# Kernel optimization log

Measured on AMD Instinct MI355X. Metric: run time of the kernel, lower is better.

## Reference

```python
import math
import jax, jax.numpy as jnp
import numpy as np

NUM_CLUSTERS = 512
KMEANS_ITERS = 3
TOLERANCE = 1e-4
N_SAMPLES = 131072
EMB_DIM = 128


def setup_inputs() -> dict:
    key = jax.random.key(0)
    data = jax.random.normal(key, (N_SAMPLES, EMB_DIM), dtype=jnp.float32)
    return {"data": data}


def _cdist(x, y):
    # Euclidean distance matrix [N, K], matching torch.cdist (p=2).
    x2 = jnp.sum(x * x, axis=-1, keepdims=True)          # [N,1]
    y2 = jnp.sum(y * y, axis=-1)                          # [K]
    sq = x2 + y2 - 2.0 * (x @ y.T)
    return jnp.sqrt(jnp.maximum(sq, 0.0))


def _assign_clusters(dist, num_clusters, max_per_cluster):
    # Capacity-constrained greedy assignment, sequential over samples
    # (faithful to the original double loop), expressed as a lax.scan.
    sorted_idx = jnp.argsort(dist, axis=-1)               # [N, K]

    def step(counts, row):
        avail = counts[row] < max_per_cluster             # [K] in preference order
        pos = jnp.argmax(avail)                           # first available cluster
        chosen = jnp.where(jnp.any(avail), row[pos], jnp.argmin(counts))
        counts = counts.at[chosen].add(1)
        return counts, chosen

    counts0 = jnp.zeros((num_clusters,), dtype=jnp.int32)
    _, labels = jax.lax.scan(step, counts0, sorted_idx)
    return labels                                         # [N] int32


def _update_codebook(data, labels, old_codebook, num_clusters):
    sums = jax.ops.segment_sum(data, labels, num_segments=num_clusters)  # [K,d]
    cnt = jax.ops.segment_sum(jnp.ones((data.shape[0],), data.dtype),
                              labels, num_segments=num_clusters)          # [K]
    means = sums / jnp.maximum(cnt, 1.0)[:, None]
    # Empty clusters keep their old centroid.
    return jnp.where(cnt[:, None] > 0, means, old_codebook)


def _fit(data):
    n, _ = data.shape
    k = NUM_CLUSTERS
    cap = math.ceil(n / k)  # static python int
    # Init: random subset of rows (num_emb >= num_clusters path).
    perm = jax.random.permutation(jax.random.key(42), n)[:k]
    codebook0 = data[perm]

    def kmeans_iter(carry, _):
        cb, labels, done = carry
        dist = _cdist(data, cb)
        new_labels = _assign_clusters(dist, k, cap)
        new_cb = _update_codebook(data, new_labels, cb, k)
        converged = jnp.linalg.norm(new_cb - cb) < TOLERANCE
        cb_out = jnp.where(done, cb, new_cb)
        labels_out = jnp.where(done, labels, new_labels)
        return (cb_out, labels_out, jnp.logical_or(done, converged)), None

    init = (codebook0, jnp.zeros((n,), jnp.int32), jnp.array(False))
    (codebook, labels, _), _ = jax.lax.scan(kmeans_iter, init, None,
                                            length=KMEANS_ITERS)
    return codebook, labels


def reference(data):
    # Returns (codebook [K,d], samples_labels [N]) like BalancedKmeans.fit.
    return _fit(data)
```

## Files before the change

kernel.cpp:

```cpp
#include <hip/hip_runtime.h>
#include <cstdint>
#include <cstring>
#include <vector>

#define RNG_PARTITIONABLE 1

#define NS 131072
#define D  128
#define KC 512
#define CAPC 256
#define TS 32

static constexpr size_t OFF_YT    = 0;
static constexpr size_t OFF_Y2    = OFF_YT + (size_t)D * KC * 8;
static constexpr size_t OFF_CB    = OFF_Y2 + (size_t)KC * 8;
static constexpr size_t OFF_NORM  = OFF_CB + (size_t)KC * D * 4;
static constexpr size_t OFF_DONE  = OFF_NORM + 8;
static constexpr size_t OFF_SCAL  = OFF_DONE + 4;
static constexpr size_t OFF_CNT   = OFF_SCAL + 12;
static constexpr size_t OFF_OPENL = OFF_CNT + (size_t)KC * 4;
static constexpr size_t OFF_MCNT  = OFF_OPENL + (size_t)KC * 2;
static constexpr size_t OFF_MEMB  = OFF_MCNT + (size_t)KC * 4;
static constexpr size_t OFF_LBL   = OFF_MEMB + (size_t)KC * CAPC * 4;
static constexpr size_t OFF_SL    = ((OFF_LBL + (size_t)NS * 4 + 15) / 16) * 16;

struct PermArg { uint32_t v[KC]; };

__device__ inline unsigned long long sortkey(double d) {
  unsigned long long u = (unsigned long long)__double_as_longlong(d);
  return (u & 0x8000000000000000ull) ? ~u : (u | 0x8000000000000000ull);
}

__device__ inline double dot128(const float* __restrict__ x, const float* __restrict__ y) {
  double s0 = 0, s1 = 0, s2 = 0, s3 = 0;
#pragma unroll
  for (int k = 0; k < D; k += 4) {
    float4 a = *reinterpret_cast<const float4*>(x + k);
    float4 b = *reinterpret_cast<const float4*>(y + k);
    s0 = fma((double)a.x, (double)b.x, s0);
    s1 = fma((double)a.y, (double)b.y, s1);
    s2 = fma((double)a.z, (double)b.z, s2);
    s3 = fma((double)a.w, (double)b.w, s3);
  }
  return (s0 + s1) + (s2 + s3);
}

__device__ inline void bitonic64(unsigned long long& k, uint32_t& v, int lane) {
#pragma unroll
  for (int sz = 2; sz <= 64; sz <<= 1) {
#pragma unroll
    for (int st = sz >> 1; st > 0; st >>= 1) {
      unsigned long long ok = __shfl_xor(k, st);
      uint32_t ov = __shfl_xor(v, st);
      bool dirAsc = ((lane & sz) == 0);
      bool low = ((lane & st) == 0);
      bool oless = (ok < k) || (ok == k && ov < v);
      bool take = (dirAsc == low) ? oless : !oless;
      if (take) { k = ok; v = ov; }
    }
  }
}

__global__ void k_init(uint32_t* done) {
  if (threadIdx.x == 0 && blockIdx.x == 0) *done = 0u;
}

__global__ void k_gather(PermArg p, const float* __restrict__ data, float* __restrict__ cb) {
  int c = blockIdx.x, t = threadIdx.x;
  cb[(size_t)c * D + t] = data[(size_t)p.v[c] * D + t];
}

__global__ __launch_bounds__(64) void k_prep(const float* __restrict__ cb,
    double* __restrict__ yT, double* __restrict__ y2g, const uint32_t* __restrict__ done) {
  if (*done) return;
  const int c = blockIdx.x;
  const int lane = threadIdx.x;
  double v0 = (double)cb[(size_t)c * D + lane];
  double v1 = (double)cb[(size_t)c * D + 64 + lane];
  yT[(size_t)lane * KC + c] = v0;
  yT[(size_t)(lane + 64) * KC + c] = v1;
  double q = fma(v0, v0, v1 * v1);
  for (int d2 = 32; d2; d2 >>= 1) q += __shfl_xor(q, d2);
  if (lane == 0) y2g[c] = q;
}

__global__ __launch_bounds__(256) void k_dist(const float* __restrict__ data,
    const double* __restrict__ yT, const double* __restrict__ y2g,
    uint16_t* __restrict__ sl, const uint32_t* __restrict__ done) {
  if (*done) return;
  __shared__ double xs[16][D];
  __shared__ uint32_t hist[256];
  __shared__ unsigned long long candK[64];
  __shared__ uint32_t candI[64];
  __shared__ uint32_t candCnt;
  __shared__ double redMn[4], redMx[4];
  __shared__ double sKey[4];
  __shared__ int sId[4];
  __shared__ int cutSh;
  __shared__ uint32_t totSh;
  __shared__ int winSh;

  const int tid = threadIdx.x;
  const int lane = tid & 63;
  const int wv = tid >> 6;
  const int rowBase = blockIdx.x * 16;

  for (int idx = tid; idx < 16 * D; idx += 256) {
    int r = idx >> 7, k = idx & 127;
    xs[r][k] = (double)data[(size_t)(rowBase + r) * D + k];
  }
  __syncthreads();

  const int c0 = tid, c1 = tid + 256;
  double acc0[16], acc1[16];
#pragma unroll
  for (int r = 0; r < 16; ++r) { acc0[r] = 0.0; acc1[r] = 0.0; }

  for (int k = 0; k < D; ++k) {
    double yv0 = yT[(size_t)k * KC + c0];
    double yv1 = yT[(size_t)k * KC + c1];
#pragma unroll
    for (int r = 0; r < 16; ++r) {
      double xv = xs[r][k];
      acc0[r] = fma(xv, yv0, acc0[r]);
      acc1[r] = fma(xv, yv1, acc1[r]);
    }
  }
  {
    double y20 = y2g[c0], y21 = y2g[c1];
#pragma unroll
    for (int r = 0; r < 16; ++r) {
      acc0[r] = fma(-2.0, acc0[r], y20);
      acc1[r] = fma(-2.0, acc1[r], y21);
    }
  }

#pragma unroll
  for (int r = 0; r < 16; ++r) {
    const double v0 = acc0[r], v1 = acc1[r];
    double mn = fmin(v0, v1), mx = fmax(v0, v1);
    for (int d2 = 32; d2; d2 >>= 1) {
      mn = fmin(mn, __shfl_xor(mn, d2));
      mx = fmax(mx, __shfl_xor(mx, d2));
    }
    if (lane == 0) { redMn[wv] = mn; redMx[wv] = mx; }
    __syncthreads();
    mn = fmin(fmin(redMn[0], redMn[1]), fmin(redMn[2], redMn[3]));
    mx = fmax(fmax(redMx[0], redMx[1]), fmax(redMx[2], redMx[3]));
    double rng = mx - mn;
    double inv = (rng > 0.0) ? (255.0 / rng) : 0.0;
    hist[tid] = 0;
    if (tid == 0) candCnt = 0;
    __syncthreads();
    int b0 = (int)((v0 - mn) * inv); b0 = b0 < 0 ? 0 : (b0 > 255 ? 255 : b0);
    int b1 = (int)((v1 - mn) * inv); b1 = b1 < 0 ? 0 : (b1 > 255 ? 255 : b1);
    atomicAdd(&hist[b0], 1u);
    atomicAdd(&hist[b1], 1u);
    __syncthreads();
    if (wv == 0) {
      uint32_t h0 = hist[lane * 4], h1 = hist[lane * 4 + 1], h2 = hist[lane * 4 + 2], h3 = hist[lane * 4 + 3];
      uint32_t ls = h0 + h1 + h2 + h3, x = ls;
      for (int d2 = 1; d2 < 64; d2 <<= 1) { uint32_t y = __shfl_up(x, d2); if (lane >= d2) x += y; }
      uint32_t e = x - ls;
      uint32_t cA = e + h0, cB = cA + h1, cC = cB + h2, cD = cC + h3;
      int mc = 999; uint32_t mt = 0;
      if (cA >= 32) { mc = lane * 4; mt = cA; }
      else if (cB >= 32) { mc = lane * 4 + 1; mt = cB; }
      else if (cC >= 32) { mc = lane * 4 + 2; mt = cC; }
      else if (cD >= 32) { mc = lane * 4 + 3; mt = cD; }
      for (int d2 = 32; d2; d2 >>= 1) {
        int oc = __shfl_xor(mc, d2); uint32_t ot = __shfl_xor(mt, d2);
        if (oc < mc) { mc = oc; mt = ot; }
      }
      if (lane == 0) { cutSh = mc; totSh = mt; }
    }
    __syncthreads();
    const int cut = cutSh;
    const uint32_t tot = totSh;
    if (tot <= 64u) {
      if (b0 <= cut) { uint32_t s2 = atomicAdd(&candCnt, 1u); candK[s2] = sortkey(v0); candI[s2] = (uint32_t)c0; }
      if (b1 <= cut) { uint32_t s2 = atomicAdd(&candCnt, 1u); candK[s2] = sortkey(v1); candI[s2] = (uint32_t)c1; }
      __syncthreads();
      if (wv == 0) {
        uint32_t nc = candCnt;
        unsigned long long kk = ~0ull; uint32_t id = 0xFFFFu;
        if ((uint32_t)lane < nc) { kk = candK[lane]; id = candI[lane]; }
        bitonic64(kk, id, lane);
        if (lane < TS) sl[(size_t)(rowBase + r) * TS + lane] = (uint16_t)id;
      }
      __syncthreads();
    } else {
      uint32_t tk = 0;
      for (int sel = 0; sel < 32; ++sel) {
        double bv = 1e300; int bc = 0x7FFFFFFF;
        if (!(tk & 1u)) { bv = v0; bc = c0; }
        if (!(tk & 2u) && (v1 < bv || (v1 == bv && c1 < bc))) { bv = v1; bc = c1; }
        for (int d2 = 32; d2; d2 >>= 1) {
          double ov = __shfl_xor(bv, d2); int oc = __shfl_xor(bc, d2);
          if (ov < bv || (ov == bv && oc < bc)) { bv = ov; bc = oc; }
        }
        if (lane == 0) { sKey[wv] = bv; sId[wv] = bc; }
        __syncthreads();
        if (tid == 0) {
          double fb = sKey[0]; int fc = sId[0];
          for (int w2 = 1; w2 < 4; ++w2) {
            if (sKey[w2] < fb || (sKey[w2] == fb && sId[w2] < fc)) { fb = sKey[w2]; fc = sId[w2]; }
          }
          winSh = fc;
          sl[(size_t)(rowBase + r) * TS + sel] = (uint16_t)fc;
        }
        __syncthreads();
        int wc = winSh;
        if (tid == (wc & 255)) tk |= (wc < 256) ? 1u : 2u;
        __syncthreads();
      }
    }
  }
}

__device__ inline int walkstep(const uint4 cc, const uint16_t* __restrict__ sl,
    uint32_t i, int& ptr, const uint32_t* cnt) {
  while (ptr < TS) {
    uint32_t c;
    if (ptr < 8) {
      uint32_t w = (ptr < 4) ? ((ptr < 2) ? cc.x : cc.y) : ((ptr < 6) ? cc.z : cc.w);
      c = (w >> ((ptr & 1) * 16)) & 0xFFFFu;
    } else {
      c = sl[(size_t)i * TS + ptr];
    }
    if (c < KC && cnt[c] < CAPC) return (int)c;
    ++ptr;
  }
  return -1;
}

__device__ inline void resolve_overflow(int& choice, uint32_t i, int lane,
    const uint32_t* cnt, const double* __restrict__ y2g,
    const float* __restrict__ cb, const float* __restrict__ data) {
  unsigned long long om = __ballot(choice < 0);
  while (om) {
    int L = __ffsll(om) - 1;
    om &= om - 1;
    uint32_t iL = __shfl(i, L);
    const float* x = data + (size_t)iL * D;
    double bv = 1e300; int bc = 0x7FFFFFFF;
    for (int j = 0; j < 8; ++j) {
      int c = lane + 64 * j;
      if (cnt[c] < CAPC) {
        double v = y2g[c] - 2.0 * dot128(x, cb + (size_t)c * D);
        if (v < bv || (v == bv && c < bc)) { bv = v; bc = c; }
      }
    }
    for (int d2 = 32; d2; d2 >>= 1) {
      double ov = __shfl_xor(bv, d2); int oc = __shfl_xor(bc, d2);
      if (ov < bv || (ov == bv && oc < bc)) { bv = ov; bc = oc; }
    }
    if (lane == L) choice = bc;
  }
}

__global__ __launch_bounds__(64) void k_ev(const float* __restrict__ data,
    const float* __restrict__ cb, const double* __restrict__ y2g,
    const uint16_t* __restrict__ sl, uint32_t* __restrict__ cntG,
    uint32_t* __restrict__ scal, uint16_t* __restrict__ openLG,
    int* __restrict__ labels, const uint32_t* __restrict__ done,
    int stopOpen, int initFlag) {
  if (*done) return;
  __shared__ uint32_t cnt[KC];
  __shared__ uint32_t hist[KC];
  __shared__ uint32_t reach[96];
  __shared__ uint32_t reachCnt;
  __shared__ uint32_t openSh;
  __shared__ uint32_t posSh;
  __shared__ uint32_t olc;
  const int lane = threadIdx.x;

  if (initFlag) {
    for (int c = lane; c < KC; c += 64) cnt[c] = 0;
    if (lane == 0) { openSh = KC; posSh = 0; }
  } else {
    for (int c = lane; c < KC; c += 64) cnt[c] = cntG[c];
    if (lane == 0) { posSh = scal[0]; openSh = scal[1]; }
  }
  __syncthreads();
  uint32_t pos = posSh;

  uint4 pf0, pf1;
  {
    uint32_t s0 = pos + lane; if (s0 >= NS) s0 = NS - 1;
    uint32_t s1 = pos + 64 + lane; if (s1 >= NS) s1 = NS - 1;
    pf0 = *reinterpret_cast<const uint4*>(sl + (size_t)s0 * TS);
    pf1 = *reinterpret_cast<const uint4*>(sl + (size_t)s1 * TS);
  }

  while (pos < NS) {
    if (openSh <= (uint32_t)stopOpen) break;
    uint32_t i = pos + lane;
    uint4 pf2;
    {
      uint32_t s2i = pos + 128 + lane; if (s2i >= NS) s2i = NS - 1;
      pf2 = *reinterpret_cast<const uint4*>(sl + (size_t)s2i * TS);
    }
    int ptr = 0;
    bool exempt = false;
    int choice = walkstep(pf0, sl, i, ptr, cnt);
    resolve_overflow(choice, i, lane, cnt, y2g, cb, data);

    for (;;) {
      for (int c = lane; c < KC; c += 64) hist[c] = 0;
      if (lane == 0) reachCnt = 0;
      __syncthreads();
      if (!exempt) atomicAdd(&hist[choice], 1u);
      __syncthreads();
      for (int c = lane; c < KC; c += 64) {
        uint32_t cc = cnt[c];
        if (cc < CAPC && cc + hist[c] >= CAPC) {
          uint32_t s2 = atomicAdd(&reachCnt, 1u);
          if (s2 < 96) reach[s2] = c;
        }
      }
      __syncthreads();
      uint32_t nr = reachCnt; if (nr > 96) nr = 96;
      if (nr == 0) break;
      int Lstar = 64;
      for (uint32_t t = 0; t < nr; ++t) {
        uint32_t c = reach[t];
        uint32_t rem = CAPC - cnt[c];
        unsigned long long m = __ballot((!exempt) && choice == (int)c);
        if ((uint32_t)__popcll(m) > rem) {
          unsigned long long mm = m;
          for (uint32_t q = 0; q < rem; ++q) mm &= mm - 1;
          int fi = __ffsll(mm) - 1;
          if (fi < Lstar) Lstar = fi;
        }
      }
      if (Lstar == 64) break;
      bool inval = false;
      for (uint32_t t = 0; t < nr; ++t) {
        uint32_t c = reach[t];
        uint32_t cc = cnt[c];
        if (cc >= CAPC) continue;
        uint32_t rem = CAPC - cc;
        unsigned long long m = __ballot((!exempt) && choice == (int)c);
        uint32_t pc = (uint32_t)__popcll(m);
        if (pc >= rem) {
          unsigned long long mm = m;
          for (uint32_t q = 0; q + 1 < rem; ++q) mm &= mm - 1;
          int fl = __ffsll(mm) - 1;
          if (fl < Lstar) {
            __syncthreads();
            if (lane == 0) { cnt[c] = CAPC; openSh--; }
            __syncthreads();
            if ((!exempt) && choice == (int)c) {
              uint32_t rk = (uint32_t)__popcll(m & ((1ull << lane) - 1ull));
              if (rk < rem) exempt = true; else inval = true;
            }
          }
        }
      }
      __syncthreads();
      if (inval) {
        if (ptr < TS) { ++ptr; choice = walkstep(pf0, sl, i, ptr, cnt); }
        else choice = -1;
      }
      resolve_overflow(choice, i, lane, cnt, y2g, cb, data);
      __syncthreads();
    }
    uint32_t old = 0;
    if (!exempt) old = atomicAdd(&cnt[choice], 1u);
    labels[i] = choice;
    __syncthreads();
    if (!exempt && old == CAPC - 1) atomicSub(&openSh, 1u);
    __syncthreads();
    pos += 64;
    pf0 = pf1; pf1 = pf2;
  }

  __syncthreads();
  for (int c = lane; c < KC; c += 64) cntG[c] = cnt[c];
  if (lane == 0) olc = 0;
  __syncthreads();
  for (int j = 0; j < 8; ++j) {
    int c = lane + 64 * j;
    bool op = cnt[c] < CAPC;
    unsigned long long m = __ballot(op);
    uint32_t base = olc;
    uint32_t rk = (uint32_t)__popcll(m & ((1ull << lane) - 1ull));
    if (op) openLG[base + rk] = (uint16_t)c;
    __syncthreads();
    if (lane == 0) olc += (uint32_t)__popcll(m);
    __syncthreads();
  }
  if (lane == 0) { scal[0] = pos; scal[1] = openSh; scal[2] = olc; }
}

__global__ __launch_bounds__(256) void k_rebuild(const float* __restrict__ data,
    const float* __restrict__ cb, const double* __restrict__ y2g,
    uint16_t* __restrict__ sl, const uint32_t* __restrict__ scal,
    const uint16_t* __restrict__ openLG, const uint32_t* __restrict__ done) {
  if (*done) return;
  uint32_t pos = scal[0];
  if (pos >= NS) return;
  uint32_t oc = scal[2]; if (oc > 64) oc = 64;
  const int lane = threadIdx.x & 63;
  const uint32_t wid = (blockIdx.x * blockDim.x + threadIdx.x) >> 6;
  const uint32_t nw = (gridDim.x * blockDim.x) >> 6;
  int c = -1; double y2v = 0.0; const float* yrow = cb;
  if ((uint32_t)lane < oc) { c = openLG[lane]; y2v = y2g[c]; yrow = cb + (size_t)c * D; }
  for (uint32_t s = pos + wid; s < NS; s += nw) {
    unsigned long long kk = ~0ull; uint32_t id = 0xFFFFu;
    if (c >= 0) {
      double v = y2v - 2.0 * dot128(data + (size_t)s * D, yrow);
      kk = sortkey(v); id = (uint32_t)c;
    }
    bitonic64(kk, id, lane);
    if (lane < TS) sl[(size_t)s * TS + lane] = (uint16_t)id;
  }
}

__global__ void k_zero(uint32_t* mcnt, double* norm) {
  int i = blockIdx.x * blockDim.x + threadIdx.x;
  if (i < KC) mcnt[i] = 0u;
  if (i == 0) *norm = 0.0;
}

__global__ void k_scatter(const int* __restrict__ labels, uint32_t* __restrict__ mcnt,
    uint32_t* __restrict__ memb, const uint32_t* __restrict__ done) {
  if (*done) return;
  uint32_t i = blockIdx.x * blockDim.x + threadIdx.x;
  int c = labels[i];
  if ((unsigned)c < KC) {
    uint32_t s = atomicAdd(&mcnt[c], 1u);
    if (s < CAPC) memb[(size_t)c * CAPC + s] = i;
  }
}

__global__ __launch_bounds__(128) void k_update(const float* __restrict__ data,
    const uint32_t* __restrict__ memb, float* __restrict__ cb,
    double* __restrict__ norm, const uint32_t* __restrict__ done) {
  if (*done) return;
  const int c = blockIdx.x, t = threadIdx.x;
  __shared__ uint32_t mem[CAPC];
  __shared__ double qq[2];
  mem[t] = memb[(size_t)c * CAPC + t] & (NS - 1);
  mem[t + 128] = memb[(size_t)c * CAPC + 128 + t] & (NS - 1);
  __syncthreads();
  double a = 0.0;
  for (int m = 0; m < CAPC; ++m) a += (double)data[(size_t)mem[m] * D + t];
  float nv = (float)(a * (1.0 / 256.0));
  double df = (double)nv - (double)cb[(size_t)c * D + t];
  cb[(size_t)c * D + t] = nv;
  double q = df * df;
  for (int d2 = 32; d2; d2 >>= 1) q += __shfl_xor(q, d2);
  if ((t & 63) == 0) qq[t >> 6] = q;
  __syncthreads();
  if (t == 0) atomicAdd(norm, qq[0] + qq[1]);
}

__global__ void k_conv(const double* __restrict__ norm, uint32_t* __restrict__ done) {
  if (threadIdx.x == 0 && blockIdx.x == 0) {
    if (*norm < 1e-8) *done = 1u;
  }
}

__global__ void k_out(const float* __restrict__ cb, float* __restrict__ o) {
  int i = blockIdx.x * blockDim.x + threadIdx.x;
  o[i] = cb[i];
}

__global__ void k_outL(const int* __restrict__ lbl, float* __restrict__ o) {
  int i = blockIdx.x * blockDim.x + threadIdx.x;
  o[i] = (float)lbl[i];
}

static void tf2x32(uint32_t k0, uint32_t k1, uint32_t x0, uint32_t x1, uint32_t& o0, uint32_t& o1) {
  uint32_t ks2 = k0 ^ k1 ^ 0x1BD11BDAu;
  x0 += k0; x1 += k1;
  auto R = [&](int r) { x0 += x1; x1 = (x1 << r) | (x1 >> (32 - r)); x1 ^= x0; };
  R(13); R(15); R(26); R(6);   x0 += k1;  x1 += ks2 + 1u;
  R(17); R(29); R(16); R(24);  x0 += ks2; x1 += k0 + 2u;
  R(13); R(15); R(26); R(6);   x0 += k0;  x1 += k1 + 3u;
  R(17); R(29); R(16); R(24);  x0 += k1;  x1 += ks2 + 4u;
  R(13); R(15); R(26); R(6);   x0 += ks2; x1 += k0 + 5u;
  o0 = x0; o1 = x1;
}

static void host_sort_kv(std::vector<uint32_t>& k, std::vector<uint32_t>& v) {
  const size_t n = k.size();
  std::vector<uint32_t> k2(n), v2(n);
  for (int sh = 0; sh < 32; sh += 8) {
    uint32_t cnt2[257];
    memset(cnt2, 0, sizeof cnt2);
    for (size_t i = 0; i < n; ++i) cnt2[((k[i] >> sh) & 255u) + 1]++;
    for (int b = 0; b < 256; ++b) cnt2[b + 1] += cnt2[b];
    for (size_t i = 0; i < n; ++i) {
      uint32_t b = (k[i] >> sh) & 255u;
      uint32_t d = cnt2[b]++;
      k2[d] = k[i]; v2[d] = v[i];
    }
    k.swap(k2); v.swap(v2);
  }
}

static void compute_perm(uint32_t* out) {
  const uint32_t n = NS;
  std::vector<uint32_t> vals(n), keys(n);
  for (uint32_t i = 0; i < n; ++i) vals[i] = i;
  uint32_t k0 = 0u, k1 = 42u;
  for (int round = 0; round < 2; ++round) {
    uint32_t nk0, nk1, sk0, sk1;
#if RNG_PARTITIONABLE
    tf2x32(k0, k1, 0u, 0u, nk0, nk1);
    tf2x32(k0, k1, 0u, 1u, sk0, sk1);
    for (uint32_t i = 0; i < n; ++i) {
      uint32_t b1, b2;
      tf2x32(sk0, sk1, 0u, i, b1, b2);
      keys[i] = b1 ^ b2;
    }
#else
    {
      uint32_t a0, b0, a1, b1v;
      tf2x32(k0, k1, 0u, 2u, a0, b0);
      tf2x32(k0, k1, 1u, 3u, a1, b1v);
      nk0 = a0; nk1 = a1; sk0 = b0; sk1 = b1v;
    }
    {
      const uint32_t h = n / 2;
      for (uint32_t i = 0; i < h; ++i) {
        uint32_t o0, o1;
        tf2x32(sk0, sk1, i, i + h, o0, o1);
        keys[i] = o0; keys[i + h] = o1;
      }
    }
#endif
    host_sort_kv(keys, vals);
    k0 = nk0; k1 = nk1;
  }
  memcpy(out, vals.data(), KC * sizeof(uint32_t));
}

extern "C" void kernel_launch(void* const* d_in, const int* in_sizes, int n_in,
                              void* d_out, int out_size, void* d_ws, size_t ws_size,
                              hipStream_t stream) {
  const float* data = (const float*)d_in[0];
  float* outCB = (float*)d_out;
  float* outLB = (float*)d_out + (size_t)KC * D;

  char* w = (char*)d_ws;
  double* yT = (double*)(w + OFF_YT);
  double* y2 = (double*)(w + OFF_Y2);
  float* cb = (float*)(w + OFF_CB);
  double* norm = (double*)(w + OFF_NORM);
  uint32_t* done = (uint32_t*)(w + OFF_DONE);
  uint32_t* scal = (uint32_t*)(w + OFF_SCAL);
  uint32_t* cnt = (uint32_t*)(w + OFF_CNT);
  uint16_t* openL = (uint16_t*)(w + OFF_OPENL);
  uint32_t* mcnt = (uint32_t*)(w + OFF_MCNT);
  uint32_t* memb = (uint32_t*)(w + OFF_MEMB);
  int* lbl = (int*)(w + OFF_LBL);
  uint16_t* sl = (uint16_t*)(w + OFF_SL);

  PermArg pa;
  compute_perm(pa.v);

  k_init<<<1, 64, 0, stream>>>(done);
  k_gather<<<KC, D, 0, stream>>>(pa, data, cb);

  for (int it = 0; it < 3; ++it) {
    k_prep<<<KC, 64, 0, stream>>>(cb, yT, y2, done);
    k_dist<<<NS / 16, 256, 0, stream>>>(data, yT, y2, sl, done);
    k_ev<<<1, 64, 0, stream>>>(data, cb, y2, sl, cnt, scal, openL, lbl, done, 64, 1);
    k_rebuild<<<256, 256, 0, stream>>>(data, cb, y2, sl, scal, openL, done);
    k_ev<<<1, 64, 0, stream>>>(data, cb, y2, sl, cnt, scal, openL, lbl, done, 32, 0);
    k_rebuild<<<256, 256, 0, stream>>>(data, cb, y2, sl, scal, openL, done);
    k_ev<<<1, 64, 0, stream>>>(data, cb, y2, sl, cnt, scal, openL, lbl, done, 0, 0);
    k_zero<<<2, 256, 0, stream>>>(mcnt, norm);
    k_scatter<<<NS / 256, 256, 0, stream>>>(lbl, mcnt, memb, done);
    k_update<<<KC, 128, 0, stream>>>(data, memb, cb, norm, done);
    k_conv<<<1, 64, 0, stream>>>(norm, done);
  }
  k_out<<<KC * D / 256, 256, 0, stream>>>(cb, outCB);
  k_outL<<<NS / 256, 256, 0, stream>>>(lbl, outLB);
}
```

Measured before the change: 125.1 ms.

## Add optimistic fast path to greedy assignment wavefront, deepen prefetch

The sequential assignment kernel now optimistically atomically adds each lane's first-available choice (unrolled check of the 8 prefetched candidates) and only falls back to the histogram/reach conflict-resolution loop if any lane overflowed capacity. Shared-memory scalars (open count, position, list offset) become wave-uniform registers updated by ballot/popcount, removing several __syncthreads per step. The sorted-list prefetch distance is increased from 2 to 5 batches ahead. It adds register pressure and relies on the rollback path being correct when overflow happens.

```diff
diff --git a/kernel.cpp b/kernel.cpp
--- a/kernel.cpp
+++ b/kernel.cpp
@@ -270,128 +270,151 @@
   __shared__ uint32_t hist[KC];
   __shared__ uint32_t reach[96];
   __shared__ uint32_t reachCnt;
-  __shared__ uint32_t openSh;
-  __shared__ uint32_t posSh;
-  __shared__ uint32_t olc;
   const int lane = threadIdx.x;
 
+  uint32_t pos, openCnt;
   if (initFlag) {
     for (int c = lane; c < KC; c += 64) cnt[c] = 0;
-    if (lane == 0) { openSh = KC; posSh = 0; }
+    pos = 0; openCnt = KC;
   } else {
     for (int c = lane; c < KC; c += 64) cnt[c] = cntG[c];
-    if (lane == 0) { posSh = scal[0]; openSh = scal[1]; }
+    pos = scal[0]; openCnt = scal[1];
   }
   __syncthreads();
-  uint32_t pos = posSh;
-
-  uint4 pf0, pf1;
+
+  uint4 p0, p1, p2, p3, p4;
   {
-    uint32_t s0 = pos + lane; if (s0 >= NS) s0 = NS - 1;
-    uint32_t s1 = pos + 64 + lane; if (s1 >= NS) s1 = NS - 1;
-    pf0 = *reinterpret_cast<const uint4*>(sl + (size_t)s0 * TS);
-    pf1 = *reinterpret_cast<const uint4*>(sl + (size_t)s1 * TS);
-  }
-
-  while (pos < NS) {
-    if (openSh <= (uint32_t)stopOpen) break;
-    uint32_t i = pos + lane;
-    uint4 pf2;
+    uint32_t s;
+    s = pos + lane;        if (s >= NS) s = NS - 1; p0 = *reinterpret_cast<const uint4*>(sl + (size_t)s * TS);
+    s = pos + 64 + lane;   if (s >= NS) s = NS - 1; p1 = *reinterpret_cast<const uint4*>(sl + (size_t)s * TS);
+    s = pos + 128 + lane;  if (s >= NS) s = NS - 1; p2 = *reinterpret_cast<const uint4*>(sl + (size_t)s * TS);
+    s = pos + 192 + lane;  if (s >= NS) s = NS - 1; p3 = *reinterpret_cast<const uint4*>(sl + (size_t)s * TS);
+    s = pos + 256 + lane;  if (s >= NS) s = NS - 1; p4 = *reinterpret_cast<const uint4*>(sl + (size_t)s * TS);
+  }
+
+  while (pos < NS && openCnt > (uint32_t)stopOpen) {
+    const uint32_t i = pos + lane;
+    uint4 pN;
     {
-      uint32_t s2i = pos + 128 + lane; if (s2i >= NS) s2i = NS - 1;
-      pf2 = *reinterpret_cast<const uint4*>(sl + (size_t)s2i * TS);
-    }
-    int ptr = 0;
-    bool exempt = false;
-    int choice = walkstep(pf0, sl, i, ptr, cnt);
+      uint32_t s = pos + 320 + lane; if (s >= NS) s = NS - 1;
+      pN = *reinterpret_cast<const uint4*>(sl + (size_t)s * TS);
+    }
+
+    uint32_t e0 = p0.x & 0xFFFFu, e1 = p0.x >> 16, e2 = p0.y & 0xFFFFu, e3 = p0.y >> 16,
+             e4 = p0.z & 0xFFFFu, e5 = p0.z >> 16, e6 = p0.w & 0xFFFFu, e7 = p0.w >> 16;
+    uint32_t q0 = cnt[e0 < KC ? e0 : 0], q1 = cnt[e1 < KC ? e1 : 0],
+             q2 = cnt[e2 < KC ? e2 : 0], q3 = cnt[e3 < KC ? e3 : 0],
+             q4 = cnt[e4 < KC ? e4 : 0], q5 = cnt[e5 < KC ? e5 : 0],
+             q6 = cnt[e6 < KC ? e6 : 0], q7 = cnt[e7 < KC ? e7 : 0];
+    int choice = -1, ptr = TS;
+    if (e7 < KC && q7 < CAPC) { choice = (int)e7; ptr = 7; }
+    if (e6 < KC && q6 < CAPC) { choice = (int)e6; ptr = 6; }
+    if (e5 < KC && q5 < CAPC) { choice = (int)e5; ptr = 5; }
+    if (e4 < KC && q4 < CAPC) { choice = (int)e4; ptr = 4; }
+    if (e3 < KC && q3 < CAPC) { choice = (int)e3; ptr = 3; }
+    if (e2 < KC && q2 < CAPC) { choice = (int)e2; ptr = 2; }
+    if (e1 < KC && q1 < CAPC) { choice = (int)e1; ptr = 1; }
+    if (e0 < KC && q0 < CAPC) { choice = (int)e0; ptr = 0; }
+    if (__ballot(choice < 0)) {
+      if (choice < 0) { ptr = 8; choice = walkstep(p0, sl, i, ptr, cnt); }
+    }
     resolve_overflow(choice, i, lane, cnt, y2g, cb, data);
 
-    for (;;) {
-      for (int c = lane; c < KC; c += 64) hist[c] = 0;
-      if (lane == 0) reachCnt = 0;
+    uint32_t old = atomicAdd(&cnt[choice], 1u);
+    unsigned long long ovf = __ballot(old >= CAPC);
+    if (ovf == 0ull) {
+      labels[i] = choice;
+      unsigned long long fills = __ballot(old == CAPC - 1);
+      openCnt -= (uint32_t)__popcll(fills);
+    } else {
+      atomicSub(&cnt[choice], 1u);
       __syncthreads();
-      if (!exempt) atomicAdd(&hist[choice], 1u);
-      __syncthreads();
-      for (int c = lane; c < KC; c += 64) {
-        uint32_t cc = cnt[c];
-        if (cc < CAPC && cc + hist[c] >= CAPC) {
-          uint32_t s2 = atomicAdd(&reachCnt, 1u);
-          if (s2 < 96) reach[s2] = c;
+      bool exempt = false;
+      for (;;) {
+        for (int c = lane; c < KC; c += 64) hist[c] = 0;
+        if (lane == 0) reachCnt = 0;
+        __syncthreads();
+        if (!exempt) atomicAdd(&hist[choice], 1u);
+        __syncthreads();
+        for (int c = lane; c < KC; c += 64) {
+          uint32_t cc = cnt[c];
+          if (cc < CAPC && cc + hist[c] >= CAPC) {
+            uint32_t s2 = atomicAdd(&reachCnt, 1u);
+            if (s2 < 96) reach[s2] = c;
+          }
         }
-      }
-      __syncthreads();
-      uint32_t nr = reachCnt; if (nr > 96) nr = 96;
-      if (nr == 0) break;
-      int Lstar = 64;
-      for (uint32_t t = 0; t < nr; ++t) {
-        uint32_t c = reach[t];
-        uint32_t rem = CAPC - cnt[c];
-        unsigned long long m = __ballot((!exempt) && choice == (int)c);
-        if ((uint32_t)__popcll(m) > rem) {
-          unsigned long long mm = m;
-          for (uint32_t q = 0; q < rem; ++q) mm &= mm - 1;
-          int fi = __ffsll(mm) - 1;
-          if (fi < Lstar) Lstar = fi;
+        __syncthreads();
+        uint32_t nr = reachCnt; if (nr > 96) nr = 96;
+        if (nr == 0) break;
+        int Lstar = 64;
+        for (uint32_t t = 0; t < nr; ++t) {
+          uint32_t c = reach[t];
+          uint32_t rem = CAPC - cnt[c];
+          unsigned long long m = __ballot((!exempt) && choice == (int)c);
+          if ((uint32_t)__popcll(m) > rem) {
+            unsigned long long mm = m;
+            for (uint32_t q = 0; q < rem; ++q) mm &= mm - 1;
+            int fi = __ffsll(mm) - 1;
+            if (fi < Lstar) Lstar = fi;
+          }
         }
-      }
-      if (Lstar == 64) break;
-      bool inval = false;
-      for (uint32_t t = 0; t < nr; ++t) {
-        uint32_t c = reach[t];
-        uint32_t cc = cnt[c];
-        if (cc >= CAPC) continue;
-        uint32_t rem = CAPC - cc;
-        unsigned long long m = __ballot((!exempt) && choice == (int)c);
-        uint32_t pc = (uint32_t)__popcll(m);
-        if (pc >= rem) {
-          unsigned long long mm = m;
-          for (uint32_t q = 0; q + 1 < rem; ++q) mm &= mm - 1;
-          int fl = __ffsll(mm) - 1;
-          if (fl < Lstar) {
-            __syncthreads();
-            if (lane == 0) { cnt[c] = CAPC; openSh--; }
-            __syncthreads();
-            if ((!exempt) && choice == (int)c) {
-              uint32_t rk = (uint32_t)__popcll(m & ((1ull << lane) - 1ull));
-              if (rk < rem) exempt = true; else inval = true;
+        if (Lstar == 64) break;
+        bool inval = false;
+        for (uint32_t t = 0; t < nr; ++t) {
+          uint32_t c = reach[t];
+          uint32_t cc = cnt[c];
+          if (cc >= CAPC) continue;
+          uint32_t rem = CAPC - cc;
+          unsigned long long m = __ballot((!exempt) && choice == (int)c);
+          uint32_t pc = (uint32_t)__popcll(m);
+          if (pc >= rem) {
+            unsigned long long mm = m;
+            for (uint32_t q = 0; q + 1 < rem; ++q) mm &= mm - 1;
+            int fl = __ffsll(mm) - 1;
+            if (fl < Lstar) {
+              __syncthreads();
+              if (lane == 0) cnt[c] = CAPC;
+              openCnt--;
+              __syncthreads();
+              if ((!exempt) && choice == (int)c) {
+                uint32_t rk = (uint32_t)__popcll(m & ((1ull << lane) - 1ull));
+                if (rk < rem) exempt = true; else inval = true;
+              }
             }
           }
         }
+        __syncthreads();
+        if (inval) {
+          if (ptr < TS) { ++ptr; choice = walkstep(p0, sl, i, ptr, cnt); }
+          else choice = -1;
+        }
+        resolve_overflow(choice, i, lane, cnt, y2g, cb, data);
+        __syncthreads();
       }
+      uint32_t oldc = 0;
+      if (!exempt) oldc = atomicAdd(&cnt[choice], 1u);
+      labels[i] = choice;
+      unsigned long long fills = __ballot((!exempt) && oldc == CAPC - 1);
+      openCnt -= (uint32_t)__popcll(fills);
       __syncthreads();
-      if (inval) {
-        if (ptr < TS) { ++ptr; choice = walkstep(pf0, sl, i, ptr, cnt); }
-        else choice = -1;
-      }
-      resolve_overflow(choice, i, lane, cnt, y2g, cb, data);
-      __syncthreads();
-    }
-    uint32_t old = 0;
-    if (!exempt) old = atomicAdd(&cnt[choice], 1u);
-    labels[i] = choice;
-    __syncthreads();
-    if (!exempt && old == CAPC - 1) atomicSub(&openSh, 1u);
-    __syncthreads();
+    }
+
     pos += 64;
-    pf0 = pf1; pf1 = pf2;
+    p0 = p1; p1 = p2; p2 = p3; p3 = p4; p4 = pN;
   }
 
   __syncthreads();
   for (int c = lane; c < KC; c += 64) cntG[c] = cnt[c];
-  if (lane == 0) olc = 0;
-  __syncthreads();
+  uint32_t base = 0;
   for (int j = 0; j < 8; ++j) {
     int c = lane + 64 * j;
     bool op = cnt[c] < CAPC;
     unsigned long long m = __ballot(op);
-    uint32_t base = olc;
     uint32_t rk = (uint32_t)__popcll(m & ((1ull << lane) - 1ull));
     if (op) openLG[base + rk] = (uint16_t)c;
-    __syncthreads();
-    if (lane == 0) olc += (uint32_t)__popcll(m);
-    __syncthreads();
-  }
-  if (lane == 0) { scal[0] = pos; scal[1] = openSh; scal[2] = olc; }
+    base += (uint32_t)__popcll(m);
+  }
+  if (lane == 0) { scal[0] = pos; scal[1] = openCnt; scal[2] = base; }
 }
 
 __global__ __launch_bounds__(256) void k_rebuild(const float* __restrict__ data,
```

Measured after the change: 121.4 ms. 1.03x faster.
